# Performance work log

Measured on AMD Instinct MI355X. Metric: run time of the kernel, lower is better.

Reference implementation:

```python
import jax, jax.numpy as jnp
import numpy as np

EPS = 1e-6

def _l2normalize(x, axis=1):
    # matches torch: x / sqrt(sum(x^2) + eps)
    norm = jnp.sqrt(jnp.sum(x * x, axis=axis, keepdims=True) + EPS)
    return x / norm


def setup_inputs() -> dict:
    key = jax.random.key(0)
    k1, k2, k3 = jax.random.split(key, 3)
    B, C, H, W = 8, 64, 48, 48
    x = jax.random.normal(k1, (B, C, H, W), dtype=jnp.float32)
    v = jax.random.normal(k2, (B, C, H, W), dtype=jnp.float32)
    pos = jax.random.normal(k3, (B, C, H, W), dtype=jnp.float32)
    # learned scalar parameters (init values from the torch module)
    gamma = jnp.float32(0.0)
    beta_gamma = jnp.float32(10.0)
    sum_gamma0 = jnp.float32(0.0)
    sum_gamma1 = jnp.float32(0.0)
    return {"x": x, "v": v, "pos": pos, "gamma": gamma,
            "beta_gamma": beta_gamma, "sum_gamma0": sum_gamma0,
            "sum_gamma1": sum_gamma1}


def reference(x, v, pos, gamma, beta_gamma, sum_gamma0, sum_gamma1):
    B, C, H, W = x.shape
    N = H * W
    # q and k are computed identically in the original module; compute once.
    q = _l2normalize(x + gamma * pos, axis=1)          # [B, C, H, W]
    qf = q.reshape(B, C, N)                             # [B, C, N]
    vf = v.reshape(B, v.shape[1], N)                    # [B, Cv, N]
    # scores[b, n, m] = <q[:, n], k[:, m]>; learned temperature beta_gamma
    scores = jnp.einsum('bcn,bcm->bnm', qf, qf) * beta_gamma  # [B, N, N]
    beta = jax.nn.softmax(scores, axis=-1)              # [B, N, N]
    # o = v @ beta^T  => o[b, c, n] = sum_m v[b, c, m] * beta[b, n, m]
    o = jnp.einsum('bcm,bnm->bcn', vf, beta).reshape(B, vf.shape[1], H, W)
    e0 = jnp.exp(sum_gamma0)
    e1 = jnp.exp(sum_gamma1)
    tot = e0 + e1
    out = (e0 / tot) * o + (e1 / tot) * v
    return out, beta.reshape(B, N, H, W)
```

## Files before the change

### kernel.cpp

```cpp
#include <hip/hip_runtime.h>
#include <hip/hip_bf16.h>

#define B_  8
#define C_  64
#define N_  2304
#define TS  64
#define NT_ (N_ / TS)
#define LDP 72
#define LDPF 68
#define SPL 4
#define MTS (NT_ / SPL)
#define BN_ (B_ * N_)

typedef __attribute__((ext_vector_type(8))) short  short8;
typedef __attribute__((ext_vector_type(4))) float  floatx4;

__device__ __forceinline__ float bf2f(unsigned short u) {
  return __uint_as_float(((unsigned int)u) << 16);
}
__device__ __forceinline__ unsigned short f2bf(float f) {
  unsigned int x = __float_as_uint(f);
  x += 0x7fff + ((x >> 16) & 1);
  return (unsigned short)(x >> 16);
}

struct Params { int f32; float gamma, bg, cmax, w0, w1; };

__device__ __forceinline__ Params load_params(const void* g, const void* bgp,
                                              const void* s0, const void* s1) {
  Params p;
  p.f32 = (((const unsigned short*)bgp)[0] == 0) ? 1 : 0;
  float sg0, sg1;
  if (p.f32) {
    p.gamma = ((const float*)g)[0];
    p.bg    = ((const float*)bgp)[0];
    sg0     = ((const float*)s0)[0];
    sg1     = ((const float*)s1)[0];
  } else {
    p.gamma = bf2f(((const unsigned short*)g)[0]);
    p.bg    = bf2f(((const unsigned short*)bgp)[0]);
    sg0     = bf2f(((const unsigned short*)s0)[0]);
    sg1     = bf2f(((const unsigned short*)s1)[0]);
  }
  float e0 = __expf(sg0), e1 = __expf(sg1);
  p.cmax = fabsf(p.bg);
  p.w0 = e0 / (e0 + e1);
  p.w1 = e1 / (e0 + e1);
  return p;
}

__global__ __launch_bounds__(256)
void prep_q(const void* __restrict__ xv, const void* __restrict__ posv,
            const void* g, const void* bgp, const void* s0p, const void* s1p,
            unsigned short* __restrict__ qT) {
  __shared__ float part[4][64];
  Params hp = load_params(g, bgp, s0p, s1p);
  int tid = threadIdx.x;
  int cg  = tid >> 6;
  int nl  = tid & 63;
  int t = blockIdx.x * 64 + nl;
  int b = t / N_;
  int n = t - b * N_;
  float gamma = hp.gamma;
  float vals[16];
  float ssq = 0.f;
  size_t base = ((size_t)(b * C_ + cg * 16)) * N_ + n;
  if (hp.f32) {
    const float* xp = (const float*)xv;
    const float* pp = (const float*)posv;
#pragma unroll
    for (int i = 0; i < 16; ++i) {
      float val = xp[base + (size_t)i * N_] + gamma * pp[base + (size_t)i * N_];
      vals[i] = val;  ssq += val * val;
    }
  } else {
    const unsigned short* xp = (const unsigned short*)xv;
    const unsigned short* pp = (const unsigned short*)posv;
#pragma unroll
    for (int i = 0; i < 16; ++i) {
      float val = bf2f(xp[base + (size_t)i * N_])
                + gamma * bf2f(pp[base + (size_t)i * N_]);
      vals[i] = val;  ssq += val * val;
    }
  }
  part[cg][nl] = ssq;
  __syncthreads();
  float s = (part[0][nl] + part[1][nl]) + (part[2][nl] + part[3][nl]);
  float inv = rsqrtf(s + 1e-6f);
  unsigned int* qrow =
      reinterpret_cast<unsigned int*>(qT + (size_t)t * C_ + cg * 16);
#pragma unroll
  for (int i = 0; i < 8; ++i) {
    qrow[i] = (unsigned int)f2bf(vals[2 * i] * inv)
            | ((unsigned int)f2bf(vals[2 * i + 1] * inv) << 16);
  }
}

__global__ __launch_bounds__(256)
void pass1_rowsum(const unsigned short* __restrict__ qT,
                  const void* __restrict__ vraw,
                  const void* g, const void* bgp, const void* s0p, const void* s1p,
                  unsigned short* __restrict__ vb,
                  float* __restrict__ rowsum_part) {
  __shared__ unsigned short qm[TS * LDP];
  Params hp = load_params(g, bgp, s0p, s1p);
  int bx  = blockIdx.x;
  int tid = threadIdx.x;
  {
    int t = bx * 256 + tid;
    unsigned int* vb32 = reinterpret_cast<unsigned int*>(vb);
    if (hp.f32) {
      const float* vf = (const float*)vraw;
#pragma unroll
      for (int k = 0; k < 2; ++k) {
        int i = t + k * 294912;
        float f0 = vf[2 * i], f1 = vf[2 * i + 1];
        vb32[i] = (unsigned int)f2bf(f0) | ((unsigned int)f2bf(f1) << 16);
      }
    } else {
      const unsigned int* v32 = (const unsigned int*)vraw;
#pragma unroll
      for (int k = 0; k < 2; ++k) {
        int i = t + k * 294912;
        vb32[i] = v32[i];
      }
    }
  }
  int s  = bx % SPL;
  int nt = (bx / SPL) % NT_;
  int b  = bx / (SPL * NT_);
  int n0 = nt * TS;
  int wave = tid >> 6;
  int lane = tid & 63;
  int quad = lane >> 4;
  int l15  = lane & 15;
  float bg = hp.bg, cmax = hp.cmax;
  const unsigned short* abase =
      qT + ((size_t)(b * N_ + n0 + 16 * wave + l15)) * C_ + quad * 8;
  short8 a0 = *reinterpret_cast<const short8*>(abase);
  short8 a1 = *reinterpret_cast<const short8*>(abase + 32);
  float acc[4] = {0.f, 0.f, 0.f, 0.f};
  int mt0 = s * MTS;
  for (int mt = mt0; mt < mt0 + MTS; ++mt) {
    int m0 = mt * TS;
    __syncthreads();
#pragma unroll
    for (int k = 0; k < 2; ++k) {
      int chunk = tid + 256 * k;
      int row = chunk >> 3;
      int col = (chunk & 7) * 8;
      short8 vv = *reinterpret_cast<const short8*>(
          qT + ((size_t)(b * N_ + m0 + row)) * C_ + col);
      *reinterpret_cast<short8*>(&qm[row * LDP + col]) = vv;
    }
    __syncthreads();
#pragma unroll
    for (int j = 0; j < 4; ++j) {
      short8 b0 = *reinterpret_cast<const short8*>(&qm[(j * 16 + l15) * LDP + quad * 8]);
      short8 b1 = *reinterpret_cast<const short8*>(&qm[(j * 16 + l15) * LDP + 32 + quad * 8]);
      floatx4 d = {0.f, 0.f, 0.f, 0.f};
      d = __builtin_amdgcn_mfma_f32_16x16x32_bf16(a0, b0, d, 0, 0, 0);
      d = __builtin_amdgcn_mfma_f32_16x16x32_bf16(a1, b1, d, 0, 0, 0);
#pragma unroll
      for (int r = 0; r < 4; ++r)
        acc[r] += __expf(fmaf(d[r], bg, -cmax));
    }
  }
#pragma unroll
  for (int r = 0; r < 4; ++r) {
    float vv = acc[r];
    vv += __shfl_xor(vv, 1);
    vv += __shfl_xor(vv, 2);
    vv += __shfl_xor(vv, 4);
    vv += __shfl_xor(vv, 8);
    acc[r] = vv;
  }
  if (l15 == 0) {
#pragma unroll
    for (int r = 0; r < 4; ++r)
      rowsum_part[(size_t)s * BN_ + b * N_ + n0 + 16 * wave + quad * 4 + r]
          = acc[r];
  }
}

__global__ __launch_bounds__(256)
void pass2_attn(const unsigned short* __restrict__ qT,
                const unsigned short* __restrict__ vb,
                const void* g, const void* bgp, const void* s0p, const void* s1p,
                const float* __restrict__ rowsum_part,
                float* __restrict__ opart,
                void* __restrict__ dout) {
  __shared__ unsigned short qm[TS * LDP];
  __shared__ float          pf[TS * LDPF];
  __shared__ unsigned short pt[TS * LDP];
  Params hp = load_params(g, bgp, s0p, s1p);
  int bx = blockIdx.x;
  int s  = bx % SPL;
  int nt = (bx / SPL) % NT_;
  int b  = bx / (SPL * NT_);
  int n0 = nt * TS;
  int tid  = threadIdx.x;
  int wave = tid >> 6;
  int lane = tid & 63;
  int quad = lane >> 4;
  int l15  = lane & 15;
  const bool f32 = hp.f32;
  float bg = hp.bg, cmax = hp.cmax;
  unsigned short* out16  = (unsigned short*)dout;
  unsigned short* beta16 = out16 + (size_t)B_ * C_ * N_;
  float* beta32 = (float*)dout + (size_t)B_ * C_ * N_;

  const unsigned short* abase =
      qT + ((size_t)(b * N_ + n0 + 16 * wave + l15)) * C_ + quad * 8;
  short8 a0 = *reinterpret_cast<const short8*>(abase);
  short8 a1 = *reinterpret_cast<const short8*>(abase + 32);
  float Ce[4];
#pragma unroll
  for (int r = 0; r < 4; ++r) {
    int row = b * N_ + n0 + 16 * wave + quad * 4 + r;
    float sum = 0.f;
#pragma unroll
    for (int ss = 0; ss < SPL; ++ss)
      sum += rowsum_part[(size_t)ss * BN_ + row];
    Ce[r] = -__logf(sum) - cmax;
  }
  floatx4 oacc[4] = {{0.f,0.f,0.f,0.f},{0.f,0.f,0.f,0.f},
                     {0.f,0.f,0.f,0.f},{0.f,0.f,0.f,0.f}};
  int mtb = s * MTS;
  const unsigned short* vrow = vb + ((size_t)(b * C_ + 16 * wave + l15)) * N_;
  int srow = tid >> 3;
  int scol = (tid & 7) * 8;
  for (int it = 0; it < MTS; ++it) {
    int m0 = (mtb + it) * TS;
    __syncthreads();
#pragma unroll
    for (int k = 0; k < 2; ++k) {
      int chunk = tid + 256 * k;
      int row = chunk >> 3;
      int col = (chunk & 7) * 8;
      short8 qv = *reinterpret_cast<const short8*>(
          qT + ((size_t)(b * N_ + m0 + row)) * C_ + col);
      *reinterpret_cast<short8*>(&qm[row * LDP + col]) = qv;
    }
    __syncthreads();
    short8 av0 = *reinterpret_cast<const short8*>(vrow + m0 + quad * 8);
    short8 av1 = *reinterpret_cast<const short8*>(vrow + m0 + 32 + quad * 8);
    if (f32) {
#pragma unroll
      for (int j = 0; j < 4; ++j) {
        short8 b0 = *reinterpret_cast<const short8*>(&qm[(j * 16 + l15) * LDP + quad * 8]);
        short8 b1 = *reinterpret_cast<const short8*>(&qm[(j * 16 + l15) * LDP + 32 + quad * 8]);
        floatx4 d = {0.f, 0.f, 0.f, 0.f};
        d = __builtin_amdgcn_mfma_f32_16x16x32_bf16(a0, b0, d, 0, 0, 0);
        d = __builtin_amdgcn_mfma_f32_16x16x32_bf16(a1, b1, d, 0, 0, 0);
#pragma unroll
        for (int r = 0; r < 4; ++r)
          pf[(16 * wave + quad * 4 + r) * LDPF + j * 16 + l15] =
              __expf(fmaf(d[r], bg, Ce[r]));
      }
      __syncthreads();
#pragma unroll
      for (int k = 0; k < 2; ++k) {
        int row = srow + 32 * k;
        const float* src = &pf[row * LDPF + scol];
        floatx4 lo = *reinterpret_cast<const floatx4*>(src);
        floatx4 hi = *reinterpret_cast<const floatx4*>(src + 4);
        short8 pk;
#pragma unroll
        for (int e = 0; e < 4; ++e) {
          pk[e]     = (short)f2bf(lo[e]);
          pk[e + 4] = (short)f2bf(hi[e]);
        }
        *reinterpret_cast<short8*>(&pt[row * LDP + scol]) = pk;
        float* dst = beta32 + ((size_t)(b * N_ + n0 + row)) * N_ + m0 + scol;
        *reinterpret_cast<floatx4*>(dst)     = lo;
        *reinterpret_cast<floatx4*>(dst + 4) = hi;
      }
      __syncthreads();
    } else {
#pragma unroll
      for (int j = 0; j < 4; ++j) {
        short8 b0 = *reinterpret_cast<const short8*>(&qm[(j * 16 + l15) * LDP + quad * 8]);
        short8 b1 = *reinterpret_cast<const short8*>(&qm[(j * 16 + l15) * LDP + 32 + quad * 8]);
        floatx4 d = {0.f, 0.f, 0.f, 0.f};
        d = __builtin_amdgcn_mfma_f32_16x16x32_bf16(a0, b0, d, 0, 0, 0);
        d = __builtin_amdgcn_mfma_f32_16x16x32_bf16(a1, b1, d, 0, 0, 0);
#pragma unroll
        for (int r = 0; r < 4; ++r)
          pt[(16 * wave + quad * 4 + r) * LDP + j * 16 + l15] =
              f2bf(__expf(fmaf(d[r], bg, Ce[r])));
      }
      __syncthreads();
#pragma unroll
      for (int k = 0; k < 2; ++k) {
        int row = srow + 32 * k;
        short8 pv = *reinterpret_cast<const short8*>(&pt[row * LDP + scol]);
        *reinterpret_cast<short8*>(
            beta16 + ((size_t)(b * N_ + n0 + row)) * N_ + m0 + scol) = pv;
      }
    }
#pragma unroll
    for (int j = 0; j < 4; ++j) {
      short8 bp0 = *reinterpret_cast<const short8*>(&pt[(j * 16 + l15) * LDP + quad * 8]);
      short8 bp1 = *reinterpret_cast<const short8*>(&pt[(j * 16 + l15) * LDP + 32 + quad * 8]);
      oacc[j] = __builtin_amdgcn_mfma_f32_16x16x32_bf16(av0, bp0, oacc[j], 0, 0, 0);
      oacc[j] = __builtin_amdgcn_mfma_f32_16x16x32_bf16(av1, bp1, oacc[j], 0, 0, 0);
    }
  }
  float* op = opart + (size_t)s * (B_ * C_ * N_);
#pragma unroll
  for (int j = 0; j < 4; ++j) {
#pragma unroll
    for (int r = 0; r < 4; ++r) {
      int c = 16 * wave + quad * 4 + r;
      int n = n0 + 16 * j + l15;
      op[((size_t)(b * C_ + c)) * N_ + n] = oacc[j][r];
    }
  }
}

__global__ __launch_bounds__(256)
void blend_k(const float* __restrict__ opart, const void* __restrict__ vraw,
             const void* g, const void* bgp, const void* s0p, const void* s1p,
             void* __restrict__ dout) {
  Params hp = load_params(g, bgp, s0p, s1p);
  int t = blockIdx.x * 256 + threadIdx.x;
  const int STR = (B_ * C_ * N_) / 4;
  const floatx4* p = reinterpret_cast<const floatx4*>(opart);
  floatx4 o = p[t];
#pragma unroll
  for (int ss = 1; ss < SPL; ++ss) {
    floatx4 q = p[t + (size_t)ss * STR];
#pragma unroll
    for (int k = 0; k < 4; ++k) o[k] += q[k];
  }
  float w0 = hp.w0, w1 = hp.w1;
  if (hp.f32) {
    floatx4 vv = reinterpret_cast<const floatx4*>(vraw)[t];
    floatx4 r;
#pragma unroll
    for (int k = 0; k < 4; ++k) r[k] = w0 * o[k] + w1 * vv[k];
    reinterpret_cast<floatx4*>(dout)[t] = r;
  } else {
    unsigned long long v64 =
        reinterpret_cast<const unsigned long long*>(vraw)[t];
    unsigned long long rr = 0;
#pragma unroll
    for (int k = 0; k < 4; ++k) {
      float vf = bf2f((unsigned short)(v64 >> (16 * k)));
      rr |= ((unsigned long long)f2bf(w0 * o[k] + w1 * vf)) << (16 * k);
    }
    reinterpret_cast<unsigned long long*>(dout)[t] = rr;
  }
}

extern "C" void kernel_launch(void* const* d_in, const int* in_sizes, int n_in,
                              void* d_out, int out_size, void* d_ws, size_t ws_size,
                              hipStream_t stream) {
  const void* x     = d_in[0];
  const void* v     = d_in[1];
  const void* pos   = d_in[2];
  const void* gamma = d_in[3];
  const void* bg    = d_in[4];
  const void* sg0   = d_in[5];
  const void* sg1   = d_in[6];

  char* ws = (char*)d_ws;
  unsigned short* qT = (unsigned short*)(ws + 256);
  unsigned short* vb = qT + (size_t)B_ * N_ * C_;
  float* rowsum_part = (float*)(ws + 256 + (size_t)B_ * N_ * C_ * 4);
  float* opart = rowsum_part + (size_t)SPL * BN_;

  prep_q<<<dim3(BN_ / 64), dim3(256), 0, stream>>>(
      x, pos, gamma, bg, sg0, sg1, qT);
  pass1_rowsum<<<dim3(B_ * NT_ * SPL), dim3(256), 0, stream>>>(
      qT, v, gamma, bg, sg0, sg1, vb, rowsum_part);
  pass2_attn<<<dim3(B_ * NT_ * SPL), dim3(256), 0, stream>>>(
      qT, vb, gamma, bg, sg0, sg1, rowsum_part, opart, d_out);
  blend_k<<<dim3((B_ * C_ * N_) / 1024), dim3(256), 0, stream>>>(
      opart, v, gamma, bg, sg0, sg1, d_out);
}
```

Baseline: 230.0 us.

## Drop separate rowsum pass by deferring softmax normalization to a final rescale

```diff
diff --git a/kernel.cpp b/kernel.cpp
--- a/kernel.cpp
+++ b/kernel.cpp
@@ -11,6 +11,9 @@
 #define SPL 4
 #define MTS (NT_ / SPL)
 #define BN_ (B_ * N_)
+
+#define NB_BLEND 1152
+#define NB_RESC  10368
 
 typedef __attribute__((ext_vector_type(8))) short  short8;
 typedef __attribute__((ext_vector_type(4))) float  floatx4;
@@ -51,11 +54,28 @@
 
 __global__ __launch_bounds__(256)
 void prep_q(const void* __restrict__ xv, const void* __restrict__ posv,
+            const void* __restrict__ vraw,
             const void* g, const void* bgp, const void* s0p, const void* s1p,
-            unsigned short* __restrict__ qT) {
+            unsigned short* __restrict__ qT, unsigned short* __restrict__ vb) {
   __shared__ float part[4][64];
   Params hp = load_params(g, bgp, s0p, s1p);
   int tid = threadIdx.x;
+  {
+    const int NU32 = (B_ * C_ * N_) / 2;
+    const int TC   = 288 * 256;
+    int t = blockIdx.x * 256 + tid;
+    unsigned int* vb32 = reinterpret_cast<unsigned int*>(vb);
+    if (hp.f32) {
+      const float* vf = (const float*)vraw;
+      for (int i = t; i < NU32; i += TC) {
+        float f0 = vf[2 * i], f1 = vf[2 * i + 1];
+        vb32[i] = (unsigned int)f2bf(f0) | ((unsigned int)f2bf(f1) << 16);
+      }
+    } else {
+      const unsigned int* v32 = (const unsigned int*)vraw;
+      for (int i = t; i < NU32; i += TC) vb32[i] = v32[i];
+    }
+  }
   int cg  = tid >> 6;
   int nl  = tid & 63;
   int t = blockIdx.x * 64 + nl;
@@ -97,97 +117,10 @@
 }
 
 __global__ __launch_bounds__(256)
-void pass1_rowsum(const unsigned short* __restrict__ qT,
-                  const void* __restrict__ vraw,
-                  const void* g, const void* bgp, const void* s0p, const void* s1p,
-                  unsigned short* __restrict__ vb,
-                  float* __restrict__ rowsum_part) {
-  __shared__ unsigned short qm[TS * LDP];
-  Params hp = load_params(g, bgp, s0p, s1p);
-  int bx  = blockIdx.x;
-  int tid = threadIdx.x;
-  {
-    int t = bx * 256 + tid;
-    unsigned int* vb32 = reinterpret_cast<unsigned int*>(vb);
-    if (hp.f32) {
-      const float* vf = (const float*)vraw;
-#pragma unroll
-      for (int k = 0; k < 2; ++k) {
-        int i = t + k * 294912;
-        float f0 = vf[2 * i], f1 = vf[2 * i + 1];
-        vb32[i] = (unsigned int)f2bf(f0) | ((unsigned int)f2bf(f1) << 16);
-      }
-    } else {
-      const unsigned int* v32 = (const unsigned int*)vraw;
-#pragma unroll
-      for (int k = 0; k < 2; ++k) {
-        int i = t + k * 294912;
-        vb32[i] = v32[i];
-      }
-    }
-  }
-  int s  = bx % SPL;
-  int nt = (bx / SPL) % NT_;
-  int b  = bx / (SPL * NT_);
-  int n0 = nt * TS;
-  int wave = tid >> 6;
-  int lane = tid & 63;
-  int quad = lane >> 4;
-  int l15  = lane & 15;
-  float bg = hp.bg, cmax = hp.cmax;
-  const unsigned short* abase =
-      qT + ((size_t)(b * N_ + n0 + 16 * wave + l15)) * C_ + quad * 8;
-  short8 a0 = *reinterpret_cast<const short8*>(abase);
-  short8 a1 = *reinterpret_cast<const short8*>(abase + 32);
-  float acc[4] = {0.f, 0.f, 0.f, 0.f};
-  int mt0 = s * MTS;
-  for (int mt = mt0; mt < mt0 + MTS; ++mt) {
-    int m0 = mt * TS;
-    __syncthreads();
-#pragma unroll
-    for (int k = 0; k < 2; ++k) {
-      int chunk = tid + 256 * k;
-      int row = chunk >> 3;
-      int col = (chunk & 7) * 8;
-      short8 vv = *reinterpret_cast<const short8*>(
-          qT + ((size_t)(b * N_ + m0 + row)) * C_ + col);
-      *reinterpret_cast<short8*>(&qm[row * LDP + col]) = vv;
-    }
-    __syncthreads();
-#pragma unroll
-    for (int j = 0; j < 4; ++j) {
-      short8 b0 = *reinterpret_cast<const short8*>(&qm[(j * 16 + l15) * LDP + quad * 8]);
-      short8 b1 = *reinterpret_cast<const short8*>(&qm[(j * 16 + l15) * LDP + 32 + quad * 8]);
-      floatx4 d = {0.f, 0.f, 0.f, 0.f};
-      d = __builtin_amdgcn_mfma_f32_16x16x32_bf16(a0, b0, d, 0, 0, 0);
-      d = __builtin_amdgcn_mfma_f32_16x16x32_bf16(a1, b1, d, 0, 0, 0);
-#pragma unroll
-      for (int r = 0; r < 4; ++r)
-        acc[r] += __expf(fmaf(d[r], bg, -cmax));
-    }
-  }
-#pragma unroll
-  for (int r = 0; r < 4; ++r) {
-    float vv = acc[r];
-    vv += __shfl_xor(vv, 1);
-    vv += __shfl_xor(vv, 2);
-    vv += __shfl_xor(vv, 4);
-    vv += __shfl_xor(vv, 8);
-    acc[r] = vv;
-  }
-  if (l15 == 0) {
-#pragma unroll
-    for (int r = 0; r < 4; ++r)
-      rowsum_part[(size_t)s * BN_ + b * N_ + n0 + 16 * wave + quad * 4 + r]
-          = acc[r];
-  }
-}
-
-__global__ __launch_bounds__(256)
-void pass2_attn(const unsigned short* __restrict__ qT,
+void pass_fused(const unsigned short* __restrict__ qT,
                 const unsigned short* __restrict__ vb,
                 const void* g, const void* bgp, const void* s0p, const void* s1p,
-                const float* __restrict__ rowsum_part,
+                float* __restrict__ rowsum_part,
                 float* __restrict__ opart,
                 void* __restrict__ dout) {
   __shared__ unsigned short qm[TS * LDP];
@@ -214,16 +147,7 @@
       qT + ((size_t)(b * N_ + n0 + 16 * wave + l15)) * C_ + quad * 8;
   short8 a0 = *reinterpret_cast<const short8*>(abase);
   short8 a1 = *reinterpret_cast<const short8*>(abase + 32);
-  float Ce[4];
-#pragma unroll
-  for (int r = 0; r < 4; ++r) {
-    int row = b * N_ + n0 + 16 * wave + quad * 4 + r;
-    float sum = 0.f;
-#pragma unroll
-    for (int ss = 0; ss < SPL; ++ss)
-      sum += rowsum_part[(size_t)ss * BN_ + row];
-    Ce[r] = -__logf(sum) - cmax;
-  }
+  float acc[4] = {0.f, 0.f, 0.f, 0.f};
   floatx4 oacc[4] = {{0.f,0.f,0.f,0.f},{0.f,0.f,0.f,0.f},
                      {0.f,0.f,0.f,0.f},{0.f,0.f,0.f,0.f}};
   int mtb = s * MTS;
@@ -254,9 +178,11 @@
         d = __builtin_amdgcn_mfma_f32_16x16x32_bf16(a0, b0, d, 0, 0, 0);
         d = __builtin_amdgcn_mfma_f32_16x16x32_bf16(a1, b1, d, 0, 0, 0);
 #pragma unroll
-        for (int r = 0; r < 4; ++r)
-          pf[(16 * wave + quad * 4 + r) * LDPF + j * 16 + l15] =
-              __expf(fmaf(d[r], bg, Ce[r]));
+        for (int r = 0; r < 4; ++r) {
+          float p = __expf(fmaf(d[r], bg, -cmax));
+          acc[r] += p;
+          pf[(16 * wave + quad * 4 + r) * LDPF + j * 16 + l15] = p;
+        }
       }
       __syncthreads();
 #pragma unroll
@@ -286,9 +212,11 @@
         d = __builtin_amdgcn_mfma_f32_16x16x32_bf16(a0, b0, d, 0, 0, 0);
         d = __builtin_amdgcn_mfma_f32_16x16x32_bf16(a1, b1, d, 0, 0, 0);
 #pragma unroll
-        for (int r = 0; r < 4; ++r)
-          pt[(16 * wave + quad * 4 + r) * LDP + j * 16 + l15] =
-              f2bf(__expf(fmaf(d[r], bg, Ce[r])));
+        for (int r = 0; r < 4; ++r) {
+          float p = __expf(fmaf(d[r], bg, -cmax));
+          acc[r] += p;
+          pt[(16 * wave + quad * 4 + r) * LDP + j * 16 + l15] = f2bf(p);
+        }
       }
       __syncthreads();
 #pragma unroll
@@ -307,6 +235,21 @@
       oacc[j] = __builtin_amdgcn_mfma_f32_16x16x32_bf16(av1, bp1, oacc[j], 0, 0, 0);
     }
   }
+#pragma unroll
+  for (int r = 0; r < 4; ++r) {
+    float vv = acc[r];
+    vv += __shfl_xor(vv, 1);
+    vv += __shfl_xor(vv, 2);
+    vv += __shfl_xor(vv, 4);
+    vv += __shfl_xor(vv, 8);
+    acc[r] = vv;
+  }
+  if (l15 == 0) {
+#pragma unroll
+    for (int r = 0; r < 4; ++r)
+      rowsum_part[(size_t)s * BN_ + b * N_ + n0 + 16 * wave + quad * 4 + r]
+          = acc[r];
+  }
   float* op = opart + (size_t)s * (B_ * C_ * N_);
 #pragma unroll
   for (int j = 0; j < 4; ++j) {
@@ -320,37 +263,87 @@
 }
 
 __global__ __launch_bounds__(256)
-void blend_k(const float* __restrict__ opart, const void* __restrict__ vraw,
+void final_k(const float* __restrict__ opart, const void* __restrict__ vraw,
              const void* g, const void* bgp, const void* s0p, const void* s1p,
+             const float* __restrict__ rowsum_part,
              void* __restrict__ dout) {
   Params hp = load_params(g, bgp, s0p, s1p);
-  int t = blockIdx.x * 256 + threadIdx.x;
-  const int STR = (B_ * C_ * N_) / 4;
-  const floatx4* p = reinterpret_cast<const floatx4*>(opart);
-  floatx4 o = p[t];
-#pragma unroll
-  for (int ss = 1; ss < SPL; ++ss) {
-    floatx4 q = p[t + (size_t)ss * STR];
-#pragma unroll
-    for (int k = 0; k < 4; ++k) o[k] += q[k];
-  }
-  float w0 = hp.w0, w1 = hp.w1;
-  if (hp.f32) {
-    floatx4 vv = reinterpret_cast<const floatx4*>(vraw)[t];
-    floatx4 r;
-#pragma unroll
-    for (int k = 0; k < 4; ++k) r[k] = w0 * o[k] + w1 * vv[k];
-    reinterpret_cast<floatx4*>(dout)[t] = r;
+  int bx = blockIdx.x;
+  int tid = threadIdx.x;
+  if (bx < NB_BLEND) {
+    int t = bx * 256 + tid;
+    const int STR = (B_ * C_ * N_) / 4;
+    const floatx4* p = reinterpret_cast<const floatx4*>(opart);
+    floatx4 o = p[t];
+#pragma unroll
+    for (int ss = 1; ss < SPL; ++ss) {
+      floatx4 q = p[t + (size_t)ss * STR];
+#pragma unroll
+      for (int k = 0; k < 4; ++k) o[k] += q[k];
+    }
+    int f = t * 4;
+    int n = f % N_;
+    int b = f / (C_ * N_);
+    int rbase = b * N_ + n;
+    floatx4 sum = {0.f, 0.f, 0.f, 0.f};
+#pragma unroll
+    for (int ss = 0; ss < SPL; ++ss) {
+      floatx4 rs = *reinterpret_cast<const floatx4*>(
+          rowsum_part + (size_t)ss * BN_ + rbase);
+#pragma unroll
+      for (int k = 0; k < 4; ++k) sum[k] += rs[k];
+    }
+    float w0 = hp.w0, w1 = hp.w1;
+    if (hp.f32) {
+      floatx4 vv = reinterpret_cast<const floatx4*>(vraw)[t];
+      floatx4 r;
+#pragma unroll
+      for (int k = 0; k < 4; ++k) r[k] = w0 * o[k] / sum[k] + w1 * vv[k];
+      reinterpret_cast<floatx4*>(dout)[t] = r;
+    } else {
+      unsigned long long v64 =
+          reinterpret_cast<const unsigned long long*>(vraw)[t];
+      unsigned long long rr = 0;
+#pragma unroll
+      for (int k = 0; k < 4; ++k) {
+        float vf = bf2f((unsigned short)(v64 >> (16 * k)));
+        rr |= ((unsigned long long)f2bf(w0 * o[k] / sum[k] + w1 * vf)) << (16 * k);
+      }
+      reinterpret_cast<unsigned long long*>(dout)[t] = rr;
+    }
   } else {
-    unsigned long long v64 =
-        reinterpret_cast<const unsigned long long*>(vraw)[t];
-    unsigned long long rr = 0;
-#pragma unroll
-    for (int k = 0; k < 4; ++k) {
-      float vf = bf2f((unsigned short)(v64 >> (16 * k)));
-      rr |= ((unsigned long long)f2bf(w0 * o[k] + w1 * vf)) << (16 * k);
-    }
-    reinterpret_cast<unsigned long long*>(dout)[t] = rr;
+    int t2 = (bx - NB_BLEND) * 256 + tid;
+    int row = t2 / 144;
+    float sum = 0.f;
+#pragma unroll
+    for (int ss = 0; ss < SPL; ++ss)
+      sum += rowsum_part[(size_t)ss * BN_ + row];
+    float inv = 1.f / sum;
+    size_t base = (size_t)t2 * 16;
+    if (hp.f32) {
+      float* beta32 = (float*)dout + (size_t)B_ * C_ * N_;
+      floatx4* pb = reinterpret_cast<floatx4*>(beta32 + base);
+#pragma unroll
+      for (int k = 0; k < 4; ++k) {
+        floatx4 vv = pb[k];
+#pragma unroll
+        for (int e = 0; e < 4; ++e) vv[e] *= inv;
+        pb[k] = vv;
+      }
+    } else {
+      unsigned short* beta16 =
+          (unsigned short*)dout + (size_t)B_ * C_ * N_ + base;
+      short8* pb = reinterpret_cast<short8*>(beta16);
+#pragma unroll
+      for (int k = 0; k < 2; ++k) {
+        short8 vv = pb[k];
+        short8 rr;
+#pragma unroll
+        for (int e = 0; e < 8; ++e)
+          rr[e] = (short)f2bf(bf2f((unsigned short)vv[e]) * inv);
+        pb[k] = rr;
+      }
+    }
   }
 }
 
@@ -372,11 +365,9 @@
   float* opart = rowsum_part + (size_t)SPL * BN_;
 
   prep_q<<<dim3(BN_ / 64), dim3(256), 0, stream>>>(
-      x, pos, gamma, bg, sg0, sg1, qT);
-  pass1_rowsum<<<dim3(B_ * NT_ * SPL), dim3(256), 0, stream>>>(
-      qT, v, gamma, bg, sg0, sg1, vb, rowsum_part);
-  pass2_attn<<<dim3(B_ * NT_ * SPL), dim3(256), 0, stream>>>(
+      x, pos, v, gamma, bg, sg0, sg1, qT, vb);
+  pass_fused<<<dim3(B_ * NT_ * SPL), dim3(256), 0, stream>>>(
       qT, vb, gamma, bg, sg0, sg1, rowsum_part, opart, d_out);
-  blend_k<<<dim3((B_ * C_ * N_) / 1024), dim3(256), 0, stream>>>(
-      opart, v, gamma, bg, sg0, sg1, d_out);
-}
+  final_k<<<dim3(NB_BLEND + NB_RESC), dim3(256), 0, stream>>>(
+      opart, v, gamma, bg, sg0, sg1, rowsum_part, d_out);
+}
```

New measurement: 272.4 us. 1.18x slower.
